# Kernel tuning notes

Measured on AMD Instinct MI355X. Metric: run time of the kernel, lower is better.

The kernel has to match this reference:

```python
import jax, jax.numpy as jnp
import numpy as np

N_NODES = 50000
N_EDGES = 800000
IN_DIM = 128
HID_DIM = 64
OUT_DIM = 40
N_REL = 8


def setup_inputs() -> dict:
    key = jax.random.key(0)
    ks = jax.random.split(key, 12)
    x = jax.random.normal(ks[0], (N_NODES, IN_DIM), dtype=jnp.float32)
    edge_index = jax.random.randint(ks[1], (2, N_EDGES), 0, N_NODES, dtype=jnp.int64)
    edge_type = jax.random.randint(ks[2], (N_EDGES,), 0, N_REL, dtype=jnp.int64)
    s = 0.05
    W1 = jax.random.normal(ks[3], (N_REL, IN_DIM, HID_DIM), dtype=jnp.float32) * s
    root1 = jax.random.normal(ks[4], (IN_DIM, HID_DIM), dtype=jnp.float32) * s
    b1 = jnp.zeros((HID_DIM,), dtype=jnp.float32)
    W2 = jax.random.normal(ks[5], (N_REL, HID_DIM, HID_DIM), dtype=jnp.float32) * s
    root2 = jax.random.normal(ks[6], (HID_DIM, HID_DIM), dtype=jnp.float32) * s
    b2 = jnp.zeros((HID_DIM,), dtype=jnp.float32)
    Wl = jax.random.normal(ks[7], (HID_DIM, OUT_DIM), dtype=jnp.float32) * s
    bl = jnp.zeros((OUT_DIM,), dtype=jnp.float32)
    return {"x": x, "edge_index": edge_index, "edge_type": edge_type,
            "W1": W1, "root1": root1, "b1": b1,
            "W2": W2, "root2": root2, "b2": b2,
            "Wl": Wl, "bl": bl}


def _rgcn_conv(x, W, Wroot, b, src, dst, edge_type):
    # PyG RGCNConv (no bases/blocks, aggr='mean'):
    #   out[i] = sum_r mean_{(j->i) of rel r} (x[j] @ W[r]) + x[i] @ Wroot + b
    N = x.shape[0]
    R = W.shape[0]
    h = jnp.einsum('ni,rio->rno', x, W)        # [R, N, out]
    msgs = h[edge_type, src]                   # [E, out] edge gather
    seg = edge_type * N + dst                  # per (relation, dst) segment
    sums = jax.ops.segment_sum(msgs, seg, num_segments=R * N)
    cnt = jax.ops.segment_sum(jnp.ones((msgs.shape[0],), x.dtype), seg,
                              num_segments=R * N)
    mean = sums / jnp.maximum(cnt, 1.0)[:, None]
    agg = mean.reshape(R, N, -1).sum(axis=0)   # sum over relations
    return agg + x @ Wroot + b


def reference(x, edge_index, edge_type, W1, root1, b1, W2, root2, b2, Wl, bl):
    src, dst = edge_index[0], edge_index[1]
    h = jax.nn.relu(_rgcn_conv(x, W1, root1, b1, src, dst, edge_type))
    # dropout is identity in eval mode
    h = jax.nn.relu(_rgcn_conv(h, W2, root2, b2, src, dst, edge_type))
    logits = h @ Wl + bl
    return jax.nn.log_softmax(logits, axis=1)
```

## Files before the change

kernel.cpp:

```cpp
#include <hip/hip_runtime.h>
#include <hip/hip_bf16.h>
#include <cmath>

#define IN_DIM 128
#define HID 64
#define OUT_DIM 40
#define NREL 8
#define NCOLS 576
#define CAP 64
#define CSTR 16

typedef __attribute__((ext_vector_type(8))) short short8;
typedef __attribute__((ext_vector_type(4))) short short4v;
typedef __attribute__((ext_vector_type(4))) float floatx4;
typedef __attribute__((ext_vector_type(2))) float f32x2;

static __device__ __forceinline__ short f2bf(float f) {
  __hip_bfloat16 h = __float2bfloat16(f);
  return __builtin_bit_cast(short, h);
}
static __device__ __forceinline__ float bflo(unsigned int u) {
  return __int_as_float(u << 16);
}
static __device__ __forceinline__ float bfhi(unsigned int u) {
  return __int_as_float(u & 0xffff0000u);
}
static __device__ __forceinline__ unsigned int packbf(float x, float y) {
  unsigned int lo = (unsigned short)f2bf(x);
  unsigned int hi = (unsigned short)f2bf(y);
  return lo | (hi << 16);
}

__global__ void pack_bt(const float* __restrict__ W1, const float* __restrict__ root1,
                        short* __restrict__ Bt1,
                        const float* __restrict__ W2, const float* __restrict__ root2,
                        short* __restrict__ Bt2) {
  const int PB1 = (NCOLS * IN_DIM + 255) / 256;
  int b = blockIdx.x;
  if (b < PB1) {
    int i = b * 256 + threadIdx.x;
    if (i >= NCOLS * IN_DIM) return;
    int c = i / IN_DIM, k = i % IN_DIM;
    float v = (c < NREL * HID)
      ? W1[((size_t)(c >> 6) * IN_DIM + k) * HID + (c & 63)]
      : root1[(size_t)k * HID + (c - NREL * HID)];
    Bt1[i] = f2bf(v);
  } else {
    int i = (b - PB1) * 256 + threadIdx.x;
    if (i >= NCOLS * HID) return;
    int c = i / HID, k = i % HID;
    float v = (c < NREL * HID)
      ? W2[((size_t)(c >> 6) * HID + k) * HID + (c & 63)]
      : root2[(size_t)k * HID + (c - NREL * HID)];
    Bt2[i] = f2bf(v);
  }
}

template<int K, int AMODE>
__device__ __forceinline__ void gemm_dev(
    short* As, short* Bs,
    const void* __restrict__ Aptr, const short* __restrict__ Bt,
    const float* __restrict__ bias, short* __restrict__ H,
    unsigned short* __restrict__ AGG, int M, int row0)
{
  constexpr int AST = K + 8;
  int tid = threadIdx.x;
  int wv = tid >> 6, lane = tid & 63;
  int lm = lane & 15, quad = lane >> 4;

  if (AMODE == 0) {
    const float* A = (const float*)Aptr;
    constexpr int CH = K / 4;
    for (int i = tid; i < 64 * CH; i += 256) {
      int r = i / CH, kq = i % CH;
      int gr = row0 + r; if (gr >= M) gr = M - 1;
      float4 v = *(const float4*)(A + (unsigned)(gr * K + kq * 4));
      short4v s;
      s.x = f2bf(v.x); s.y = f2bf(v.y); s.z = f2bf(v.z); s.w = f2bf(v.w);
      *(short4v*)(As + r * AST + kq * 4) = s;
    }
  } else {
    const short* A = (const short*)Aptr;
    constexpr int CH = K / 8;
    for (int i = tid; i < 64 * CH; i += 256) {
      int r = i / CH, ko = i % CH;
      int gr = row0 + r; if (gr >= M) gr = M - 1;
      short8 v = *(const short8*)(A + (unsigned)(gr * K + ko * 8));
      #pragma unroll
      for (int j = 0; j < 8; ++j)
        if ((unsigned short)v[j] & 0x8000u) v[j] = 0;
      *(short8*)(As + r * AST + ko * 8) = v;
    }
  }

  const short* ap = As + (16 * wv + lm) * AST + quad * 8;

  for (int cy = 0; cy < 9; ++cy) {
    constexpr int CB = K / 8;
    for (int i = tid; i < 64 * CB; i += 256) {
      int n = i / CB, ko = i % CB;
      short8 v = *(const short8*)(Bt + (unsigned)((cy * 64 + n) * K + ko * 8));
      *(short8*)(Bs + n * AST + ko * 8) = v;
    }
    __syncthreads();

    floatx4 acc[4] = {{0,0,0,0},{0,0,0,0},{0,0,0,0},{0,0,0,0}};
    #pragma unroll
    for (int ks = 0; ks < K / 32; ++ks) {
      short8 a = *(const short8*)(ap + ks * 32);
      #pragma unroll
      for (int nb = 0; nb < 4; ++nb) {
        short8 b = *(const short8*)(Bs + (nb * 16 + lm) * AST + ks * 32 + quad * 8);
        acc[nb] = __builtin_amdgcn_mfma_f32_16x16x32_bf16(a, b, acc[nb], 0, 0, 0);
      }
    }
    __syncthreads();

    int mbase = row0 + 16 * wv + quad * 4;
    if (cy < 8) {
      #pragma unroll
      for (int nb = 0; nb < 4; ++nb) {
        int col = cy * 64 + nb * 16 + lm;
        #pragma unroll
        for (int r = 0; r < 4; ++r) {
          int mg = mbase + r;
          if (mg < M) H[(unsigned)mg * (NREL * HID) + col] = f2bf(acc[nb][r]);
        }
      }
    } else {
      #pragma unroll
      for (int nb = 0; nb < 4; ++nb) {
        int col = nb * 16 + lm;
        float bv = bias[col];
        #pragma unroll
        for (int r = 0; r < 4; ++r) {
          int mg = mbase + r;
          if (mg < M)
            AGG[(unsigned)mg * HID + col] = (unsigned short)f2bf(acc[nb][r] + bv);
        }
      }
    }
  }
}

__global__ __launch_bounds__(256, 4) void gemm1_scatter(
    const float* __restrict__ A, const short* __restrict__ Bt,
    const float* __restrict__ bias, short* __restrict__ H,
    unsigned short* __restrict__ AGG, int M, int GB,
    const int* __restrict__ src, const int* __restrict__ dst,
    const int* __restrict__ et,
    int* __restrict__ cursor, int* __restrict__ ev, int E)
{
  constexpr int AST = IN_DIM + 8;
  __shared__ short As[64 * AST];
  __shared__ short Bs[64 * AST];
  if ((int)blockIdx.x < GB) {
    gemm_dev<IN_DIM, 0>(As, Bs, A, Bt, bias, H, AGG, M, blockIdx.x * 64);
  } else {
    int e = (blockIdx.x - GB) * 256 + threadIdx.x;
    if (e >= E) return;
    int d = dst[e];
    int pos = atomicAdd(&cursor[d * CSTR], 1);
    if (pos < CAP)
      __builtin_nontemporal_store((src[e] << 3) | et[e], &ev[d * CAP + pos]);
  }
}

__global__ __launch_bounds__(256, 4) void gemm2_mfma(
    const unsigned short* __restrict__ A, const short* __restrict__ Bt,
    const float* __restrict__ bias, short* __restrict__ H,
    unsigned short* __restrict__ AGG, int M)
{
  constexpr int AST = HID + 8;
  __shared__ short As[64 * AST];
  __shared__ short Bs[64 * AST];
  gemm_dev<HID, 1>(As, Bs, A, Bt, bias, H, AGG, M, blockIdx.x * 64);
}

__global__ __launch_bounds__(256) void finalize_ev(
    const int* __restrict__ cursor, int* __restrict__ ev, int N)
{
  int d = blockIdx.x * 4 + (threadIdx.x >> 6);
  if (d >= N) return;
  int lane = threadIdx.x & 63;
  int cnt = cursor[d * CSTR]; if (cnt > CAP) cnt = CAP;
  int e = (lane < cnt) ? ev[d * CAP + lane] : 0;
  int t = e & 7;
  int code = 64;
  #pragma unroll
  for (int r = 0; r < 8; ++r) {
    unsigned long long m = __ballot(lane < cnt && t == r);
    int c = __popcll(m);
    if (lane < cnt && t == r) code = c - 1;
  }
  ev[d * CAP + lane] = (lane < cnt) ? ((e << 7) | code) : 64;
}

static __device__ __forceinline__ void agg_half(
    const uint2* __restrict__ Hu2, const int* __restrict__ evrow,
    int npass, int qloc, int sub, const float* __restrict__ lut,
    float& a0, float& a1, float& a2, float& a3)
{
  f32x2 A01 = {a0, a1}, A23 = {a2, a3};
  for (int P = 0; P < npass; ++P) {
    const int4* pp = (const int4*)(evrow + P * 16 + qloc * 8);
    int4 v0 = pp[0], v1 = pp[1];
    int vv[8] = {v0.x, v0.y, v0.z, v0.w, v1.x, v1.y, v1.z, v1.w};
    uint2 hv[8];
    float ww[8];
    #pragma unroll
    for (int i = 0; i < 8; ++i) {
      hv[i] = Hu2[(unsigned)(vv[i] >> 7) * 16u + (unsigned)sub];
      ww[i] = lut[vv[i] & 127];
    }
    #pragma unroll
    for (int i = 0; i < 8; ++i) {
      f32x2 w2 = {ww[i], ww[i]};
      f32x2 h01 = {bflo(hv[i].x), bfhi(hv[i].x)};
      f32x2 h23 = {bflo(hv[i].y), bfhi(hv[i].y)};
      A01 += h01 * w2;
      A23 += h23 * w2;
    }
  }
  a0 = A01.x; a1 = A01.y; a2 = A23.x; a3 = A23.y;
  a0 += __shfl_xor(a0, 16, 64);
  a1 += __shfl_xor(a1, 16, 64);
  a2 += __shfl_xor(a2, 16, 64);
  a3 += __shfl_xor(a3, 16, 64);
}

__global__ __launch_bounds__(256) void csr_agg(
    const short* __restrict__ H, const int* __restrict__ cursor,
    const int* __restrict__ ev, unsigned short* __restrict__ AGG, int N)
{
  __shared__ float lut[128];
  int tid = threadIdx.x;
  if (tid < 128) lut[tid] = (tid < 64) ? 1.0f / (float)(tid + 1) : 0.f;
  __syncthreads();

  int wv = tid >> 6, lane = tid & 63;
  int h = lane >> 5, lhl = lane & 31, qloc = lhl >> 4, sub = lhl & 15;
  int d = blockIdx.x * 8 + wv * 2 + h;
  if (d >= N) return;

  int cnt = cursor[d * CSTR]; if (cnt > CAP) cnt = CAP;
  float a0 = 0.f, a1 = 0.f, a2 = 0.f, a3 = 0.f;
  uint2* aggrow = (uint2*)(AGG + (size_t)d * HID);
  if (qloc == 0) {
    uint2 iv = aggrow[sub];
    a0 = bflo(iv.x); a1 = bfhi(iv.x); a2 = bflo(iv.y); a3 = bfhi(iv.y);
  }
  int npass = (cnt + 15) >> 4;
  if (npass > 0)
    agg_half((const uint2*)H, ev + d * CAP, npass, qloc, sub, lut, a0, a1, a2, a3);
  if (qloc == 0) {
    uint2 ov;
    ov.x = packbf(a0, a1);
    ov.y = packbf(a2, a3);
    aggrow[sub] = ov;
  }
}

__global__ __launch_bounds__(256) void csr_agg_final(
    const short* __restrict__ H, const int* __restrict__ cursor,
    const int* __restrict__ ev, const unsigned short* __restrict__ AGG,
    const float* __restrict__ Wl, const float* __restrict__ bl,
    float* __restrict__ out, int N)
{
  __shared__ float sWl[HID * OUT_DIM];
  __shared__ float sbl[OUT_DIM];
  __shared__ float sh[8][HID];
  __shared__ float lut[128];
  int tid = threadIdx.x;
  int wv = tid >> 6, lane = tid & 63;
  int h = lane >> 5, lhl = lane & 31, qloc = lhl >> 4, sub = lhl & 15;
  int d = blockIdx.x * 8 + wv * 2 + h;
  int dc = d < N ? d : N - 1;

  int cnt = cursor[dc * CSTR]; if (cnt > CAP) cnt = CAP;
  uint2 iv = ((const uint2*)(AGG + (size_t)dc * HID))[sub];

  for (int i = tid; i < HID * OUT_DIM; i += 256) sWl[i] = Wl[i];
  if (tid < OUT_DIM) sbl[tid] = bl[tid];
  if (tid < 128) lut[tid] = (tid < 64) ? 1.0f / (float)(tid + 1) : 0.f;
  __syncthreads();

  float a0 = 0.f, a1 = 0.f, a2 = 0.f, a3 = 0.f;
  if (qloc == 0) {
    a0 = bflo(iv.x); a1 = bfhi(iv.x); a2 = bflo(iv.y); a3 = bfhi(iv.y);
  }
  int npass = (cnt + 15) >> 4;
  if (npass > 0)
    agg_half((const uint2*)H, ev + dc * CAP, npass, qloc, sub, lut, a0, a1, a2, a3);
  if (qloc == 0) {
    float4 v;
    v.x = fmaxf(a0, 0.f); v.y = fmaxf(a1, 0.f);
    v.z = fmaxf(a2, 0.f); v.w = fmaxf(a3, 0.f);
    *(float4*)(&sh[wv * 2 + h][4 * sub]) = v;
  }
  __syncthreads();

  #pragma unroll
  for (int ii = 0; ii < 2; ++ii) {
    int dd = blockIdx.x * 8 + wv * 2 + ii;
    const float* row = sh[wv * 2 + ii];
    float logit = -__builtin_inff();
    if (lane < OUT_DIM) {
      float t = sbl[lane];
      #pragma unroll 8
      for (int k = 0; k < HID; ++k) t += row[k] * sWl[k * OUT_DIM + lane];
      logit = t;
    }
    float m = logit;
    #pragma unroll
    for (int o = 32; o > 0; o >>= 1) m = fmaxf(m, __shfl_xor(m, o, 64));
    float ex = (lane < OUT_DIM) ? expf(logit - m) : 0.f;
    float s = ex;
    #pragma unroll
    for (int o = 32; o > 0; o >>= 1) s += __shfl_xor(s, o, 64);
    if (dd < N && lane < OUT_DIM)
      out[(size_t)dd * OUT_DIM + lane] = logit - m - logf(s);
  }
}

extern "C" void kernel_launch(void* const* d_in, const int* in_sizes, int n_in,
                              void* d_out, int out_size, void* d_ws, size_t ws_size,
                              hipStream_t stream) {
  const float* x     = (const float*)d_in[0];
  const int*   eidx  = (const int*)d_in[1];
  const int*   etype = (const int*)d_in[2];
  const float* W1    = (const float*)d_in[3];
  const float* root1 = (const float*)d_in[4];
  const float* b1    = (const float*)d_in[5];
  const float* W2    = (const float*)d_in[6];
  const float* root2 = (const float*)d_in[7];
  const float* b2    = (const float*)d_in[8];
  const float* Wl    = (const float*)d_in[9];
  const float* bl    = (const float*)d_in[10];

  int N = in_sizes[0] / IN_DIM;
  int E = in_sizes[2];
  const int* srcp = eidx;
  const int* dstp = eidx + E;

  char* ws = (char*)d_ws;
  size_t off = 0;
  auto alloc = [&](size_t bytes) -> char* {
    char* p = ws + off;
    off += (bytes + 255) & ~(size_t)255;
    return p;
  };
  short* Bt1    = (short*)alloc((size_t)NCOLS * IN_DIM * 2);
  short* Bt2    = (short*)alloc((size_t)NCOLS * HID * 2);
  int*   cursor = (int*)alloc((size_t)N * CSTR * 4);
  int*   ev     = (int*)alloc((size_t)N * CAP * 4);
  short* H1     = (short*)alloc((size_t)N * NREL * HID * 2);
  short* H2     = (short*)alloc((size_t)N * NREL * HID * 2);
  unsigned short* AGG1 = (unsigned short*)alloc((size_t)N * HID * 2);
  unsigned short* AGG2 = (unsigned short*)alloc((size_t)N * HID * 2);

  hipMemsetAsync(cursor, 0, (size_t)N * CSTR * 4, stream);

  const int PB1 = (NCOLS * IN_DIM + 255) / 256;
  const int PB2 = (NCOLS * HID + 255) / 256;
  pack_bt<<<PB1 + PB2, 256, 0, stream>>>(W1, root1, Bt1, W2, root2, Bt2);

  int GB = (N + 63) / 64;
  int SB = (E + 255) / 256;
  gemm1_scatter<<<GB + SB, 256, 0, stream>>>(x, Bt1, b1, H1, AGG1, N, GB,
                                             srcp, dstp, etype, cursor, ev, E);

  finalize_ev<<<(N + 3) / 4, 256, 0, stream>>>(cursor, ev, N);

  csr_agg<<<(N + 7) / 8, 256, 0, stream>>>(H1, cursor, ev, AGG1, N);

  gemm2_mfma<<<GB, 256, 0, stream>>>(AGG1, Bt2, b2, H2, AGG2, N);

  csr_agg_final<<<(N + 7) / 8, 256, 0, stream>>>(H2, cursor, ev, AGG2,
                                                 Wl, bl, (float*)d_out, N);
}
```

Measured before the change: 227.1 us.

## Make CSR aggregation kernels persistent with next-node metadata prefetch

```diff
diff --git a/kernel.cpp b/kernel.cpp
--- a/kernel.cpp
+++ b/kernel.cpp
@@ -9,6 +9,7 @@
 #define NCOLS 576
 #define CAP 64
 #define CSTR 16
+#define AGB 2048
 
 typedef __attribute__((ext_vector_type(8))) short short8;
 typedef __attribute__((ext_vector_type(4))) short short4v;
@@ -196,42 +197,32 @@
   ev[d * CAP + lane] = (lane < cnt) ? ((e << 7) | code) : 64;
 }
 
-static __device__ __forceinline__ void agg_half(
-    const uint2* __restrict__ Hu2, const int* __restrict__ evrow,
-    int npass, int qloc, int sub, const float* __restrict__ lut,
-    float& a0, float& a1, float& a2, float& a3)
-{
-  f32x2 A01 = {a0, a1}, A23 = {a2, a3};
-  for (int P = 0; P < npass; ++P) {
-    const int4* pp = (const int4*)(evrow + P * 16 + qloc * 8);
-    int4 v0 = pp[0], v1 = pp[1];
-    int vv[8] = {v0.x, v0.y, v0.z, v0.w, v1.x, v1.y, v1.z, v1.w};
-    uint2 hv[8];
-    float ww[8];
-    #pragma unroll
-    for (int i = 0; i < 8; ++i) {
-      hv[i] = Hu2[(unsigned)(vv[i] >> 7) * 16u + (unsigned)sub];
-      ww[i] = lut[vv[i] & 127];
-    }
-    #pragma unroll
-    for (int i = 0; i < 8; ++i) {
-      f32x2 w2 = {ww[i], ww[i]};
-      f32x2 h01 = {bflo(hv[i].x), bfhi(hv[i].x)};
-      f32x2 h23 = {bflo(hv[i].y), bfhi(hv[i].y)};
-      A01 += h01 * w2;
-      A23 += h23 * w2;
-    }
-  }
-  a0 = A01.x; a1 = A01.y; a2 = A23.x; a3 = A23.y;
-  a0 += __shfl_xor(a0, 16, 64);
-  a1 += __shfl_xor(a1, 16, 64);
-  a2 += __shfl_xor(a2, 16, 64);
-  a3 += __shfl_xor(a3, 16, 64);
+static __device__ __forceinline__ void agg_pass(
+    const uint2* __restrict__ Hu2, int4 v0, int4 v1, int sub,
+    const float* __restrict__ lut, f32x2& A01, f32x2& A23)
+{
+  int vv[8] = {v0.x, v0.y, v0.z, v0.w, v1.x, v1.y, v1.z, v1.w};
+  uint2 hv[8];
+  float ww[8];
+  #pragma unroll
+  for (int i = 0; i < 8; ++i) {
+    hv[i] = Hu2[(unsigned)(vv[i] >> 7) * 16u + (unsigned)sub];
+    ww[i] = lut[vv[i] & 127];
+  }
+  #pragma unroll
+  for (int i = 0; i < 8; ++i) {
+    f32x2 w2 = {ww[i], ww[i]};
+    f32x2 h01 = {bflo(hv[i].x), bfhi(hv[i].x)};
+    f32x2 h23 = {bflo(hv[i].y), bfhi(hv[i].y)};
+    A01 += h01 * w2;
+    A23 += h23 * w2;
+  }
 }
 
 __global__ __launch_bounds__(256) void csr_agg(
     const short* __restrict__ H, const int* __restrict__ cursor,
-    const int* __restrict__ ev, unsigned short* __restrict__ AGG, int N)
+    const int* __restrict__ ev, unsigned short* __restrict__ AGG,
+    int N, int nwaves)
 {
   __shared__ float lut[128];
   int tid = threadIdx.x;
@@ -240,24 +231,53 @@
 
   int wv = tid >> 6, lane = tid & 63;
   int h = lane >> 5, lhl = lane & 31, qloc = lhl >> 4, sub = lhl & 15;
-  int d = blockIdx.x * 8 + wv * 2 + h;
-  if (d >= N) return;
-
-  int cnt = cursor[d * CSTR]; if (cnt > CAP) cnt = CAP;
-  float a0 = 0.f, a1 = 0.f, a2 = 0.f, a3 = 0.f;
-  uint2* aggrow = (uint2*)(AGG + (size_t)d * HID);
-  if (qloc == 0) {
-    uint2 iv = aggrow[sub];
-    a0 = bflo(iv.x); a1 = bfhi(iv.x); a2 = bflo(iv.y); a3 = bfhi(iv.y);
-  }
-  int npass = (cnt + 15) >> 4;
-  if (npass > 0)
-    agg_half((const uint2*)H, ev + d * CAP, npass, qloc, sub, lut, a0, a1, a2, a3);
-  if (qloc == 0) {
-    uint2 ov;
-    ov.x = packbf(a0, a1);
-    ov.y = packbf(a2, a3);
-    aggrow[sub] = ov;
+  int wid = blockIdx.x * 4 + wv;
+  int stride = nwaves * 2;
+  const uint2* Hu2 = (const uint2*)H;
+
+  int dbase = wid * 2;
+  int d = dbase + h;
+  int dc = d < N ? d : N - 1;
+  int cnt = cursor[dc * CSTR]; if (cnt > CAP) cnt = CAP;
+  int4 p0 = *(const int4*)(ev + dc * CAP + qloc * 8);
+  int4 p1 = *(const int4*)(ev + dc * CAP + qloc * 8 + 4);
+  uint2 iv = ((const uint2*)(AGG + (size_t)dc * HID))[sub];
+
+  while (dbase < N) {
+    int dbn = dbase + stride;
+    int dn = dbn + h;
+    int dnc = dn < N ? dn : N - 1;
+    int cnt_n = cursor[dnc * CSTR]; if (cnt_n > CAP) cnt_n = CAP;
+    int4 q0 = *(const int4*)(ev + dnc * CAP + qloc * 8);
+    int4 q1 = *(const int4*)(ev + dnc * CAP + qloc * 8 + 4);
+    uint2 ivn = ((const uint2*)(AGG + (size_t)dnc * HID))[sub];
+
+    f32x2 A01 = {0.f, 0.f}, A23 = {0.f, 0.f};
+    if (qloc == 0) {
+      A01.x = bflo(iv.x); A01.y = bfhi(iv.x);
+      A23.x = bflo(iv.y); A23.y = bfhi(iv.y);
+    }
+    int npass = (cnt + 15) >> 4;
+    if (npass > 0) agg_pass(Hu2, p0, p1, sub, lut, A01, A23);
+    for (int P = 1; P < npass; ++P) {
+      int4 r0 = *(const int4*)(ev + dc * CAP + P * 16 + qloc * 8);
+      int4 r1 = *(const int4*)(ev + dc * CAP + P * 16 + qloc * 8 + 4);
+      agg_pass(Hu2, r0, r1, sub, lut, A01, A23);
+    }
+    float a0 = A01.x, a1 = A01.y, a2 = A23.x, a3 = A23.y;
+    a0 += __shfl_xor(a0, 16, 64);
+    a1 += __shfl_xor(a1, 16, 64);
+    a2 += __shfl_xor(a2, 16, 64);
+    a3 += __shfl_xor(a3, 16, 64);
+    if (d < N && qloc == 0) {
+      uint2 ov;
+      ov.x = packbf(a0, a1);
+      ov.y = packbf(a2, a3);
+      ((uint2*)(AGG + (size_t)d * HID))[sub] = ov;
+    }
+
+    dbase = dbn; d = dn; dc = dnc;
+    cnt = cnt_n; p0 = q0; p1 = q1; iv = ivn;
   }
 }
 
@@ -265,61 +285,88 @@
     const short* __restrict__ H, const int* __restrict__ cursor,
     const int* __restrict__ ev, const unsigned short* __restrict__ AGG,
     const float* __restrict__ Wl, const float* __restrict__ bl,
-    float* __restrict__ out, int N)
+    float* __restrict__ out, int N, int nwaves)
 {
   __shared__ float sWl[HID * OUT_DIM];
   __shared__ float sbl[OUT_DIM];
   __shared__ float sh[8][HID];
   __shared__ float lut[128];
   int tid = threadIdx.x;
-  int wv = tid >> 6, lane = tid & 63;
-  int h = lane >> 5, lhl = lane & 31, qloc = lhl >> 4, sub = lhl & 15;
-  int d = blockIdx.x * 8 + wv * 2 + h;
-  int dc = d < N ? d : N - 1;
-
-  int cnt = cursor[dc * CSTR]; if (cnt > CAP) cnt = CAP;
-  uint2 iv = ((const uint2*)(AGG + (size_t)dc * HID))[sub];
-
   for (int i = tid; i < HID * OUT_DIM; i += 256) sWl[i] = Wl[i];
   if (tid < OUT_DIM) sbl[tid] = bl[tid];
   if (tid < 128) lut[tid] = (tid < 64) ? 1.0f / (float)(tid + 1) : 0.f;
   __syncthreads();
 
-  float a0 = 0.f, a1 = 0.f, a2 = 0.f, a3 = 0.f;
-  if (qloc == 0) {
-    a0 = bflo(iv.x); a1 = bfhi(iv.x); a2 = bflo(iv.y); a3 = bfhi(iv.y);
-  }
-  int npass = (cnt + 15) >> 4;
-  if (npass > 0)
-    agg_half((const uint2*)H, ev + dc * CAP, npass, qloc, sub, lut, a0, a1, a2, a3);
-  if (qloc == 0) {
-    float4 v;
-    v.x = fmaxf(a0, 0.f); v.y = fmaxf(a1, 0.f);
-    v.z = fmaxf(a2, 0.f); v.w = fmaxf(a3, 0.f);
-    *(float4*)(&sh[wv * 2 + h][4 * sub]) = v;
-  }
-  __syncthreads();
-
-  #pragma unroll
-  for (int ii = 0; ii < 2; ++ii) {
-    int dd = blockIdx.x * 8 + wv * 2 + ii;
-    const float* row = sh[wv * 2 + ii];
-    float logit = -__builtin_inff();
-    if (lane < OUT_DIM) {
-      float t = sbl[lane];
-      #pragma unroll 8
-      for (int k = 0; k < HID; ++k) t += row[k] * sWl[k * OUT_DIM + lane];
-      logit = t;
-    }
-    float m = logit;
+  int wv = tid >> 6, lane = tid & 63;
+  int h = lane >> 5, lhl = lane & 31, qloc = lhl >> 4, sub = lhl & 15;
+  int wid = blockIdx.x * 4 + wv;
+  int stride = nwaves * 2;
+  const uint2* Hu2 = (const uint2*)H;
+
+  int dbase = wid * 2;
+  int d = dbase + h;
+  int dc = d < N ? d : N - 1;
+  int cnt = cursor[dc * CSTR]; if (cnt > CAP) cnt = CAP;
+  int4 p0 = *(const int4*)(ev + dc * CAP + qloc * 8);
+  int4 p1 = *(const int4*)(ev + dc * CAP + qloc * 8 + 4);
+  uint2 iv = ((const uint2*)(AGG + (size_t)dc * HID))[sub];
+
+  while (dbase < N) {
+    int dbn = dbase + stride;
+    int dn = dbn + h;
+    int dnc = dn < N ? dn : N - 1;
+    int cnt_n = cursor[dnc * CSTR]; if (cnt_n > CAP) cnt_n = CAP;
+    int4 q0 = *(const int4*)(ev + dnc * CAP + qloc * 8);
+    int4 q1 = *(const int4*)(ev + dnc * CAP + qloc * 8 + 4);
+    uint2 ivn = ((const uint2*)(AGG + (size_t)dnc * HID))[sub];
+
+    f32x2 A01 = {0.f, 0.f}, A23 = {0.f, 0.f};
+    if (qloc == 0) {
+      A01.x = bflo(iv.x); A01.y = bfhi(iv.x);
+      A23.x = bflo(iv.y); A23.y = bfhi(iv.y);
+    }
+    int npass = (cnt + 15) >> 4;
+    if (npass > 0) agg_pass(Hu2, p0, p1, sub, lut, A01, A23);
+    for (int P = 1; P < npass; ++P) {
+      int4 r0 = *(const int4*)(ev + dc * CAP + P * 16 + qloc * 8);
+      int4 r1 = *(const int4*)(ev + dc * CAP + P * 16 + qloc * 8 + 4);
+      agg_pass(Hu2, r0, r1, sub, lut, A01, A23);
+    }
+    float a0 = A01.x, a1 = A01.y, a2 = A23.x, a3 = A23.y;
+    a0 += __shfl_xor(a0, 16, 64);
+    a1 += __shfl_xor(a1, 16, 64);
+    a2 += __shfl_xor(a2, 16, 64);
+    a3 += __shfl_xor(a3, 16, 64);
+    if (qloc == 0) {
+      float4 v;
+      v.x = fmaxf(a0, 0.f); v.y = fmaxf(a1, 0.f);
+      v.z = fmaxf(a2, 0.f); v.w = fmaxf(a3, 0.f);
+      *(float4*)(&sh[wv * 2 + h][4 * sub]) = v;
+    }
     #pragma unroll
-    for (int o = 32; o > 0; o >>= 1) m = fmaxf(m, __shfl_xor(m, o, 64));
-    float ex = (lane < OUT_DIM) ? expf(logit - m) : 0.f;
-    float s = ex;
-    #pragma unroll
-    for (int o = 32; o > 0; o >>= 1) s += __shfl_xor(s, o, 64);
-    if (dd < N && lane < OUT_DIM)
-      out[(size_t)dd * OUT_DIM + lane] = logit - m - logf(s);
+    for (int ii = 0; ii < 2; ++ii) {
+      int dd = dbase + ii;
+      const float* row = sh[wv * 2 + ii];
+      float logit = -__builtin_inff();
+      if (lane < OUT_DIM) {
+        float t = sbl[lane];
+        #pragma unroll 8
+        for (int k = 0; k < HID; ++k) t += row[k] * sWl[k * OUT_DIM + lane];
+        logit = t;
+      }
+      float m = logit;
+      #pragma unroll
+      for (int o = 32; o > 0; o >>= 1) m = fmaxf(m, __shfl_xor(m, o, 64));
+      float ex = (lane < OUT_DIM) ? expf(logit - m) : 0.f;
+      float s = ex;
+      #pragma unroll
+      for (int o = 32; o > 0; o >>= 1) s += __shfl_xor(s, o, 64);
+      if (dd < N && lane < OUT_DIM)
+        out[(size_t)dd * OUT_DIM + lane] = logit - m - logf(s);
+    }
+
+    dbase = dbn; d = dn; dc = dnc;
+    cnt = cnt_n; p0 = q0; p1 = q1; iv = ivn;
   }
 }
 
@@ -372,10 +419,10 @@
 
   finalize_ev<<<(N + 3) / 4, 256, 0, stream>>>(cursor, ev, N);
 
-  csr_agg<<<(N + 7) / 8, 256, 0, stream>>>(H1, cursor, ev, AGG1, N);
+  csr_agg<<<AGB, 256, 0, stream>>>(H1, cursor, ev, AGG1, N, AGB * 4);
 
   gemm2_mfma<<<GB, 256, 0, stream>>>(AGG1, Bt2, b2, H2, AGG2, N);
 
-  csr_agg_final<<<(N + 7) / 8, 256, 0, stream>>>(H2, cursor, ev, AGG2,
-                                                 Wl, bl, (float*)d_out, N);
-}
+  csr_agg_final<<<AGB, 256, 0, stream>>>(H2, cursor, ev, AGG2,
+                                         Wl, bl, (float*)d_out, N, AGB * 4);
+}
```

Result: slower. 234.9 us (+3.4%).
